# Kernel tuning notes

Hardware: AMD Instinct MI355X
Metric: run time of the kernel (lower is better)

## Reference

```python
import jax, jax.numpy as jnp
import numpy as np

NEG_BIG = -1e12
ALPHA = 0.2  # LeakyReLU negative slope

def setup_inputs() -> dict:
    key = jax.random.key(0)
    k1, k2, k3, k4, k5 = jax.random.split(key, 5)
    N, F_in, F_out = 8192, 256, 128
    inp = jax.random.normal(k1, (N, F_in), dtype=jnp.float32)
    adj = jax.random.randint(k2, (N, N), 0, 2, dtype=jnp.int32)
    W = jax.random.normal(k3, (F_in, F_out), dtype=jnp.float32) * 0.05
    W_2 = jax.random.normal(k4, (F_in, F_out), dtype=jnp.float32) * 0.05
    W_3 = jax.random.normal(k5, (F_in, F_out), dtype=jnp.float32) * 0.05
    return {"inp": inp, "adj": adj, "W": W, "W_2": W_2, "W_3": W_3}

def reference(inp, adj, W, W_2, W_3):
    # h = inp @ W, h_2 = inp @ W_2  -> scores e = LeakyReLU(h @ h_2^T)  [N, N]
    h = inp @ W
    h_2 = inp @ W_2
    e = jax.nn.leaky_relu(h @ h_2.T, negative_slope=ALPHA)
    # adjacency mask, row softmax (dropout disabled: eval mode)
    attention = jax.nn.softmax(jnp.where(adj > 0, e, NEG_BIG), axis=1)
    h_3 = inp @ W_3
    h_prime = attention @ h_3
    return jax.nn.elu(h_prime)  # concat=True path
```

## Files before the change

kernel.cpp:

```cpp
#include <hip/hip_runtime.h>
#include <hip/hip_fp16.h>

#define N    8192
#define FIN  256
#define FOUT 128
#define BN   64

typedef _Float16 half8 __attribute__((ext_vector_type(8)));
typedef _Float16 half4v __attribute__((ext_vector_type(4)));
typedef float floatx4 __attribute__((ext_vector_type(4)));

__global__ __launch_bounds__(256)
void wprep_kernel(const float* __restrict__ W0,
                  const float* __restrict__ W1,
                  const float* __restrict__ W2,
                  _Float16* __restrict__ Wf)
{
    int idx  = blockIdx.x * 256 + threadIdx.x;
    int lane = idx & 63;
    int frag = idx >> 6;
    int w    = frag >> 6;
    int f    = frag & 63;
    int nt   = f >> 3, kc = f & 7;
    int quad = lane >> 4, lo16 = lane & 15;
    const float* Wp = w == 0 ? W0 : (w == 1 ? W1 : W2);
    half8 v;
#pragma unroll
    for (int jj = 0; jj < 8; jj++)
        v[jj] = (_Float16)Wp[(size_t)(kc * 32 + quad * 8 + jj) * FOUT + nt * 16 + lo16];
    *(half8*)&Wf[(size_t)idx * 8] = v;
}

__global__ __launch_bounds__(256, 2)
void gemm3_kernel(const float* __restrict__ inp,
                  const _Float16* __restrict__ Wf,
                  _Float16* __restrict__ H,
                  _Float16* __restrict__ H2,
                  _Float16* __restrict__ H3T)
{
    const int which = blockIdx.z;
    const int c0    = blockIdx.y * 64;
    const _Float16* Wfw = Wf + (size_t)which * 64 * 64 * 8;
    const int r0 = blockIdx.x * 64;
    const int tid  = threadIdx.x;
    const int wave = tid >> 6;
    const int lane = tid & 63;
    const int lo16 = lane & 15;
    const int quad = lane >> 4;
    const int r = r0 + wave * 16 + lo16;

    half8 a[8];
#pragma unroll
    for (int kc = 0; kc < 8; kc++) {
        const float* p = &inp[(size_t)r * FIN + kc * 32 + quad * 8];
        float4 v0 = *(const float4*)p;
        float4 v1 = *(const float4*)(p + 4);
        a[kc][0] = (_Float16)v0.x; a[kc][1] = (_Float16)v0.y;
        a[kc][2] = (_Float16)v0.z; a[kc][3] = (_Float16)v0.w;
        a[kc][4] = (_Float16)v1.x; a[kc][5] = (_Float16)v1.y;
        a[kc][6] = (_Float16)v1.z; a[kc][7] = (_Float16)v1.w;
    }

    floatx4 acc[4];
#pragma unroll
    for (int i = 0; i < 4; i++) acc[i] = (floatx4){0.f, 0.f, 0.f, 0.f};

#pragma unroll
    for (int kc = 0; kc < 8; kc++)
#pragma unroll
        for (int nt = 0; nt < 4; nt++) {
            int ntg = (c0 >> 4) + nt;
            half8 b = *(const half8*)&Wfw[(((size_t)ntg * 8 + kc) * 64 + lane) * 8];
            acc[nt] = __builtin_amdgcn_mfma_f32_16x16x32_f16(a[kc], b, acc[nt], 0, 0, 0);
        }

    const int arow = wave * 16 + quad * 4;
    if (which < 2) {
        _Float16* outp = which == 0 ? H : H2;
#pragma unroll
        for (int nt = 0; nt < 4; nt++)
#pragma unroll
            for (int rr = 0; rr < 4; rr++)
                outp[(size_t)(r0 + arow + rr) * FOUT + c0 + nt * 16 + lo16] = (_Float16)acc[nt][rr];
    } else {
#pragma unroll
        for (int nt = 0; nt < 4; nt++) {
            half4v v;
#pragma unroll
            for (int rr = 0; rr < 4; rr++) v[rr] = (_Float16)acc[nt][rr];
            *(half4v*)&H3T[(size_t)(c0 + nt * 16 + lo16) * N + r0 + arow] = v;
        }
    }
}

__global__ __launch_bounds__(256)
void repackK_kernel(const _Float16* __restrict__ H2, _Float16* __restrict__ Kf)
{
    int idx  = blockIdx.x * 256 + threadIdx.x;
    int lane = idx & 63;
    int frag = idx >> 6;
    int jb = frag >> 4, f = frag & 15;
    int c = f >> 3, ntj = (f >> 2) & 1, kc = f & 3;
    int quad = lane >> 4, lo16 = lane & 15;
    int srcrow = jb * 64 + c * 32 + (lo16 >> 2) * 8 + ntj * 4 + (lo16 & 3);
    half8 v = *(const half8*)&H2[(size_t)srcrow * FOUT + kc * 32 + quad * 8];
    *(half8*)&Kf[(size_t)idx * 8] = v;
}

__global__ __launch_bounds__(256)
void repackV_kernel(const _Float16* __restrict__ H3T, _Float16* __restrict__ Vf)
{
    int idx  = blockIdx.x * 256 + threadIdx.x;
    int lane = idx & 63;
    int frag = idx >> 6;
    int jb = frag >> 4, f = frag & 15, nt = f >> 1, kc = f & 1;
    int quad = lane >> 4, lo16 = lane & 15;
    half8 v = *(const half8*)&H3T[(size_t)(nt * 16 + lo16) * N + jb * 64 + kc * 32 + quad * 8];
    *(half8*)&Vf[(size_t)idx * 8] = v;
}

template<int JS>
__global__ __launch_bounds__(256, 2)
void attn_kernel(const _Float16* __restrict__ Hq,
                 const _Float16* __restrict__ Kf,
                 const _Float16* __restrict__ Vf,
                 const int* __restrict__ adj,
                 float* __restrict__ OpartT,
                 float* __restrict__ mpart,
                 float* __restrict__ lpart)
{
    __shared__ _Float16 KV[2][16384];

    const int tid  = threadIdx.x;
    const int wave = tid >> 6;
    const int lane = tid & 63;
    const int lo16 = lane & 15;
    const int quad = lane >> 4;
    const int bid  = blockIdx.x;
    const int js   = bid & (JS - 1);
    const int ib   = bid / JS;
    const int i0   = ib * 128;
    const int iw   = i0 + wave * 32;
    const int jbeg = js * (N / JS);
    const int NIT  = (N / JS) / BN;

    half8 q[2][4];
#pragma unroll
    for (int isub = 0; isub < 2; isub++)
#pragma unroll
        for (int kc = 0; kc < 4; kc++)
            q[isub][kc] = *(const half8*)&Hq[(size_t)(iw + isub * 16 + lo16) * FOUT + kc * 32 + quad * 8];

    floatx4 O[8][2];
#pragma unroll
    for (int nt = 0; nt < 8; nt++)
#pragma unroll
        for (int s = 0; s < 2; s++) O[nt][s] = (floatx4){0.f, 0.f, 0.f, 0.f};
    float m_s[2] = {-1e12f, -1e12f}, l_s[2] = {0.f, 0.f};

    int av[32];
    {
        const int* ap = adj + (size_t)iw * N + jbeg + lane;
#pragma unroll
        for (int x = 0; x < 32; x++) av[x] = ap[(size_t)x * N];
    }

    {
        const int jb0 = jbeg >> 6;
        const _Float16* gk = Kf + (size_t)jb0 * 8192;
        const _Float16* gv = Vf + (size_t)jb0 * 8192;
#pragma unroll
        for (int r = 0; r < 4; r++) {
            int off = (r * 256 + tid) * 8;
            *(half8*)&KV[0][off]        = *(const half8*)&gk[off];
            *(half8*)&KV[0][8192 + off] = *(const half8*)&gv[off];
        }
        __syncthreads();
    }

    int cur = 0;
    for (int it = 0; it < NIT; it++) {
        const int j0 = jbeg + it * BN;

        unsigned long long mw0 = 0, mw1 = 0;
#pragma unroll
        for (int x = 0; x < 16; x++) {
            unsigned long long b0 = __ballot(av[x] != 0);
            unsigned long long b1 = __ballot(av[x + 16] != 0);
            bool sel = (lo16 == x);
            mw0 = sel ? b0 : mw0;
            mw1 = sel ? b1 : mw1;
        }
        unsigned long long mw[2] = {mw0, mw1};

        if (it + 1 < NIT) {
            const int* ap = adj + (size_t)iw * N + (j0 + BN) + lane;
#pragma unroll
            for (int x = 0; x < 32; x++) av[x] = ap[(size_t)x * N];
        }

        half8 st[8];
        if (it + 1 < NIT) {
            const int jbn = (j0 + BN) >> 6;
            const _Float16* gk = Kf + (size_t)jbn * 8192;
            const _Float16* gv = Vf + (size_t)jbn * 8192;
#pragma unroll
            for (int r = 0; r < 4; r++) {
                int off = (r * 256 + tid) * 8;
                st[r]     = *(const half8*)&gk[off];
                st[r + 4] = *(const half8*)&gv[off];
            }
        }

        const _Float16* kb = &KV[cur][0];
        const _Float16* vb = &KV[cur][8192];

        floatx4 S[2][2][2];
#pragma unroll
        for (int c = 0; c < 2; c++)
#pragma unroll
            for (int ntj = 0; ntj < 2; ntj++) {
                S[c][ntj][0] = (floatx4){0.f, 0.f, 0.f, 0.f};
                S[c][ntj][1] = (floatx4){0.f, 0.f, 0.f, 0.f};
#pragma unroll
                for (int kc = 0; kc < 4; kc++) {
                    half8 kf = *(const half8*)&kb[(((c * 2 + ntj) * 4 + kc) * 64 + lane) * 8];
                    S[c][ntj][0] = __builtin_amdgcn_mfma_f32_16x16x32_f16(kf, q[0][kc], S[c][ntj][0], 0, 0, 0);
                    S[c][ntj][1] = __builtin_amdgcn_mfma_f32_16x16x32_f16(kf, q[1][kc], S[c][ntj][1], 0, 0, 0);
                }
            }

        float alpha[2];
#pragma unroll
        for (int s = 0; s < 2; s++) {
            float mx = -1e12f;
#pragma unroll
            for (int c = 0; c < 2; c++)
#pragma unroll
                for (int ntj = 0; ntj < 2; ntj++)
#pragma unroll
                    for (int r = 0; r < 4; r++) {
                        float e = S[c][ntj][s][r];
                        e = e > 0.f ? e : 0.2f * e;
                        mx = fmaxf(mx, e);
                    }
            mx = fmaxf(mx, __shfl_xor(mx, 16));
            mx = fmaxf(mx, __shfl_xor(mx, 32));
            float mn = fmaxf(m_s[s], mx);
            alpha[s] = __expf(m_s[s] - mn);
            m_s[s] = mn;
        }

        half8 pb[2][2];
        float sum[2] = {0.f, 0.f};
#pragma unroll
        for (int s = 0; s < 2; s++) {
            unsigned long long mq = mw[s] >> (quad * 8);
#pragma unroll
            for (int c = 0; c < 2; c++)
#pragma unroll
                for (int ntj = 0; ntj < 2; ntj++)
#pragma unroll
                    for (int r = 0; r < 4; r++) {
                        float e = S[c][ntj][s][r];
                        e = e > 0.f ? e : 0.2f * e;
                        bool bit = (mq >> (c * 32 + ntj * 4 + r)) & 1ull;
                        float p = bit ? __expf(e - m_s[s]) : 0.f;
                        sum[s] += p;
                        pb[s][c][ntj * 4 + r] = (_Float16)p;
                    }
            sum[s] += __shfl_xor(sum[s], 16);
            sum[s] += __shfl_xor(sum[s], 32);
            l_s[s] = l_s[s] * alpha[s] + sum[s];
#pragma unroll
            for (int nt = 0; nt < 8; nt++)
#pragma unroll
                for (int r = 0; r < 4; r++)
                    O[nt][s][r] *= alpha[s];
        }

#pragma unroll
        for (int c = 0; c < 2; c++)
#pragma unroll
            for (int nt = 0; nt < 8; nt++) {
                half8 vf = *(const half8*)&vb[((nt * 2 + c) * 64 + lane) * 8];
                O[nt][0] = __builtin_amdgcn_mfma_f32_16x16x32_f16(vf, pb[0][c], O[nt][0], 0, 0, 0);
                O[nt][1] = __builtin_amdgcn_mfma_f32_16x16x32_f16(vf, pb[1][c], O[nt][1], 0, 0, 0);
            }

        if (it + 1 < NIT) {
            const int nxt = cur ^ 1;
#pragma unroll
            for (int r = 0; r < 4; r++) {
                int off = (r * 256 + tid) * 8;
                *(half8*)&KV[nxt][off]        = st[r];
                *(half8*)&KV[nxt][8192 + off] = st[r + 4];
            }
        }
        __syncthreads();
        cur ^= 1;
    }

#pragma unroll
    for (int nt = 0; nt < 8; nt++)
#pragma unroll
        for (int s = 0; s < 2; s++)
#pragma unroll
            for (int r = 0; r < 4; r++) {
                int f = nt * 16 + quad * 4 + r;
                int i = iw + s * 16 + lo16;
                OpartT[((size_t)js * FOUT + f) * N + i] = O[nt][s][r];
            }
    if (quad == 0) {
#pragma unroll
        for (int s = 0; s < 2; s++) {
            mpart[js * N + iw + s * 16 + lo16] = m_s[s];
            lpart[js * N + iw + s * 16 + lo16] = l_s[s];
        }
    }
}

template<int JS>
__global__ __launch_bounds__(256)
void combine_kernel(const float* __restrict__ OpartT,
                    const float* __restrict__ mpart,
                    const float* __restrict__ lpart,
                    float* __restrict__ out)
{
    int idx = blockIdx.x * 256 + threadIdx.x;
    int f  = idx >> 11;
    int i4 = (idx & 2047) << 2;

    float4 M = {-3e38f, -3e38f, -3e38f, -3e38f};
    float4 m[JS];
#pragma unroll
    for (int s = 0; s < JS; s++) {
        m[s] = *(const float4*)&mpart[s * N + i4];
        M.x = fmaxf(M.x, m[s].x); M.y = fmaxf(M.y, m[s].y);
        M.z = fmaxf(M.z, m[s].z); M.w = fmaxf(M.w, m[s].w);
    }
    float4 L = {0.f, 0.f, 0.f, 0.f};
    float4 w[JS];
#pragma unroll
    for (int s = 0; s < JS; s++) {
        float4 l = *(const float4*)&lpart[s * N + i4];
        w[s].x = __expf(m[s].x - M.x); w[s].y = __expf(m[s].y - M.y);
        w[s].z = __expf(m[s].z - M.z); w[s].w = __expf(m[s].w - M.w);
        L.x += l.x * w[s].x; L.y += l.y * w[s].y;
        L.z += l.z * w[s].z; L.w += l.w * w[s].w;
    }
    float4 o = {0.f, 0.f, 0.f, 0.f};
#pragma unroll
    for (int s = 0; s < JS; s++) {
        float4 v = *(const float4*)&OpartT[((size_t)s * FOUT + f) * N + i4];
        o.x += w[s].x * v.x; o.y += w[s].y * v.y;
        o.z += w[s].z * v.z; o.w += w[s].w * v.w;
    }
    float r0 = o.x / L.x, r1 = o.y / L.y, r2 = o.z / L.z, r3 = o.w / L.w;
    out[(size_t)(i4 + 0) * FOUT + f] = r0 > 0.f ? r0 : __expf(r0) - 1.f;
    out[(size_t)(i4 + 1) * FOUT + f] = r1 > 0.f ? r1 : __expf(r1) - 1.f;
    out[(size_t)(i4 + 2) * FOUT + f] = r2 > 0.f ? r2 : __expf(r2) - 1.f;
    out[(size_t)(i4 + 3) * FOUT + f] = r3 > 0.f ? r3 : __expf(r3) - 1.f;
}

extern "C" void kernel_launch(void* const* d_in, const int* in_sizes, int n_in,
                              void* d_out, int out_size, void* d_ws, size_t ws_size,
                              hipStream_t stream) {
    const float* inp = (const float*)d_in[0];
    const int*   adj = (const int*)d_in[1];
    const float* W0  = (const float*)d_in[2];
    const float* W1  = (const float*)d_in[3];
    const float* W2  = (const float*)d_in[4];
    float* out = (float*)d_out;

    constexpr int JS = 8;
    char* ws = (char*)d_ws;
    _Float16* H    = (_Float16*)(ws);
    _Float16* H2   = (_Float16*)(ws + (2u << 20));
    _Float16* H3T  = (_Float16*)(ws + (4u << 20));
    _Float16* Wf   = (_Float16*)(ws + (6u << 20));
    _Float16* Kf   = (_Float16*)(ws + (7u << 20));
    _Float16* Vf   = (_Float16*)(ws + (9u << 20));
    float* OpartT  = (float*)(ws + (11u << 20));
    float* mpart   = (float*)(ws + (43u << 20));
    float* lpart   = (float*)(ws + (43u << 20) + (size_t)JS * N * sizeof(float));

    wprep_kernel<<<48, 256, 0, stream>>>(W0, W1, W2, Wf);
    gemm3_kernel<<<dim3(N / 64, 2, 3), 256, 0, stream>>>(inp, Wf, H, H2, H3T);
    repackK_kernel<<<512, 256, 0, stream>>>(H2, Kf);
    repackV_kernel<<<512, 256, 0, stream>>>(H3T, Vf);
    attn_kernel<JS><<<(N / 128) * JS, 256, 0, stream>>>(H, Kf, Vf, adj, OpartT, mpart, lpart);
    combine_kernel<JS><<<(FOUT * (N / 4)) / 256, 256, 0, stream>>>(OpartT, mpart, lpart, out);
}
```

Baseline: 428.5 us.

## Split attention tile into two 32-column sub-steps and merge repack kernels

The attention inner loop now handles each 64-column key block as two 32-column halves. Each half runs its own online-softmax update and PV MFMA, so fewer score registers are live at once, which eases register pressure at two blocks per SM. The adjacency prefetch is moved after the K/V global loads, and the two repack kernels are merged into one launch. The cost is twice as many max/sum reductions and O rescales per block.

```diff
diff --git a/kernel.cpp b/kernel.cpp
--- a/kernel.cpp
+++ b/kernel.cpp
@@ -94,29 +94,30 @@
 }
 
 __global__ __launch_bounds__(256)
-void repackK_kernel(const _Float16* __restrict__ H2, _Float16* __restrict__ Kf)
-{
-    int idx  = blockIdx.x * 256 + threadIdx.x;
-    int lane = idx & 63;
-    int frag = idx >> 6;
-    int jb = frag >> 4, f = frag & 15;
-    int c = f >> 3, ntj = (f >> 2) & 1, kc = f & 3;
-    int quad = lane >> 4, lo16 = lane & 15;
-    int srcrow = jb * 64 + c * 32 + (lo16 >> 2) * 8 + ntj * 4 + (lo16 & 3);
-    half8 v = *(const half8*)&H2[(size_t)srcrow * FOUT + kc * 32 + quad * 8];
-    *(half8*)&Kf[(size_t)idx * 8] = v;
-}
-
-__global__ __launch_bounds__(256)
-void repackV_kernel(const _Float16* __restrict__ H3T, _Float16* __restrict__ Vf)
-{
-    int idx  = blockIdx.x * 256 + threadIdx.x;
-    int lane = idx & 63;
-    int frag = idx >> 6;
-    int jb = frag >> 4, f = frag & 15, nt = f >> 1, kc = f & 1;
-    int quad = lane >> 4, lo16 = lane & 15;
-    half8 v = *(const half8*)&H3T[(size_t)(nt * 16 + lo16) * N + jb * 64 + kc * 32 + quad * 8];
-    *(half8*)&Vf[(size_t)idx * 8] = v;
+void repackKV_kernel(const _Float16* __restrict__ H2,
+                     const _Float16* __restrict__ H3T,
+                     _Float16* __restrict__ Kf,
+                     _Float16* __restrict__ Vf)
+{
+    if (blockIdx.x < 512) {
+        int idx  = blockIdx.x * 256 + threadIdx.x;
+        int lane = idx & 63;
+        int frag = idx >> 6;
+        int jb = frag >> 4, f = frag & 15;
+        int c = f >> 3, ntj = (f >> 2) & 1, kc = f & 3;
+        int quad = lane >> 4, lo16 = lane & 15;
+        int srcrow = jb * 64 + c * 32 + (lo16 >> 2) * 8 + ntj * 4 + (lo16 & 3);
+        half8 v = *(const half8*)&H2[(size_t)srcrow * FOUT + kc * 32 + quad * 8];
+        *(half8*)&Kf[(size_t)idx * 8] = v;
+    } else {
+        int idx  = (blockIdx.x - 512) * 256 + threadIdx.x;
+        int lane = idx & 63;
+        int frag = idx >> 6;
+        int jb = frag >> 4, f = frag & 15, nt = f >> 1, kc = f & 1;
+        int quad = lane >> 4, lo16 = lane & 15;
+        half8 v = *(const half8*)&H3T[(size_t)(nt * 16 + lo16) * N + jb * 64 + kc * 32 + quad * 8];
+        *(half8*)&Vf[(size_t)idx * 8] = v;
+    }
 }
 
 template<int JS>
@@ -193,12 +194,6 @@
         }
         unsigned long long mw[2] = {mw0, mw1};
 
-        if (it + 1 < NIT) {
-            const int* ap = adj + (size_t)iw * N + (j0 + BN) + lane;
-#pragma unroll
-            for (int x = 0; x < 32; x++) av[x] = ap[(size_t)x * N];
-        }
-
         half8 st[8];
         if (it + 1 < NIT) {
             const int jbn = (j0 + BN) >> 6;
@@ -212,81 +207,82 @@
             }
         }
 
+        if (it + 1 < NIT) {
+            const int* ap = adj + (size_t)iw * N + (j0 + BN) + lane;
+#pragma unroll
+            for (int x = 0; x < 32; x++) av[x] = ap[(size_t)x * N];
+        }
+
         const _Float16* kb = &KV[cur][0];
         const _Float16* vb = &KV[cur][8192];
 
-        floatx4 S[2][2][2];
-#pragma unroll
-        for (int c = 0; c < 2; c++)
+#pragma unroll
+        for (int c = 0; c < 2; c++) {
+            floatx4 S[2][2];
 #pragma unroll
             for (int ntj = 0; ntj < 2; ntj++) {
-                S[c][ntj][0] = (floatx4){0.f, 0.f, 0.f, 0.f};
-                S[c][ntj][1] = (floatx4){0.f, 0.f, 0.f, 0.f};
+                S[ntj][0] = (floatx4){0.f, 0.f, 0.f, 0.f};
+                S[ntj][1] = (floatx4){0.f, 0.f, 0.f, 0.f};
 #pragma unroll
                 for (int kc = 0; kc < 4; kc++) {
                     half8 kf = *(const half8*)&kb[(((c * 2 + ntj) * 4 + kc) * 64 + lane) * 8];
-                    S[c][ntj][0] = __builtin_amdgcn_mfma_f32_16x16x32_f16(kf, q[0][kc], S[c][ntj][0], 0, 0, 0);
-                    S[c][ntj][1] = __builtin_amdgcn_mfma_f32_16x16x32_f16(kf, q[1][kc], S[c][ntj][1], 0, 0, 0);
+                    S[ntj][0] = __builtin_amdgcn_mfma_f32_16x16x32_f16(kf, q[0][kc], S[ntj][0], 0, 0, 0);
+                    S[ntj][1] = __builtin_amdgcn_mfma_f32_16x16x32_f16(kf, q[1][kc], S[ntj][1], 0, 0, 0);
                 }
             }
 
-        float alpha[2];
-#pragma unroll
-        for (int s = 0; s < 2; s++) {
-            float mx = -1e12f;
-#pragma unroll
-            for (int c = 0; c < 2; c++)
+            float alpha[2];
+#pragma unroll
+            for (int s = 0; s < 2; s++) {
+                float mx = -1e12f;
 #pragma unroll
                 for (int ntj = 0; ntj < 2; ntj++)
 #pragma unroll
                     for (int r = 0; r < 4; r++) {
-                        float e = S[c][ntj][s][r];
+                        float e = S[ntj][s][r];
                         e = e > 0.f ? e : 0.2f * e;
                         mx = fmaxf(mx, e);
                     }
-            mx = fmaxf(mx, __shfl_xor(mx, 16));
-            mx = fmaxf(mx, __shfl_xor(mx, 32));
-            float mn = fmaxf(m_s[s], mx);
-            alpha[s] = __expf(m_s[s] - mn);
-            m_s[s] = mn;
-        }
-
-        half8 pb[2][2];
-        float sum[2] = {0.f, 0.f};
-#pragma unroll
-        for (int s = 0; s < 2; s++) {
-            unsigned long long mq = mw[s] >> (quad * 8);
-#pragma unroll
-            for (int c = 0; c < 2; c++)
+                mx = fmaxf(mx, __shfl_xor(mx, 16));
+                mx = fmaxf(mx, __shfl_xor(mx, 32));
+                float mn = fmaxf(m_s[s], mx);
+                alpha[s] = __expf(m_s[s] - mn);
+                m_s[s] = mn;
+            }
+
+            half8 pb[2];
+            float sum[2] = {0.f, 0.f};
+#pragma unroll
+            for (int s = 0; s < 2; s++) {
+                unsigned long long mq = mw[s] >> (quad * 8 + c * 32);
 #pragma unroll
                 for (int ntj = 0; ntj < 2; ntj++)
 #pragma unroll
                     for (int r = 0; r < 4; r++) {
-                        float e = S[c][ntj][s][r];
+                        float e = S[ntj][s][r];
                         e = e > 0.f ? e : 0.2f * e;
-                        bool bit = (mq >> (c * 32 + ntj * 4 + r)) & 1ull;
+                        bool bit = (mq >> (ntj * 4 + r)) & 1ull;
                         float p = bit ? __expf(e - m_s[s]) : 0.f;
                         sum[s] += p;
-                        pb[s][c][ntj * 4 + r] = (_Float16)p;
+                        pb[s][ntj * 4 + r] = (_Float16)p;
                     }
-            sum[s] += __shfl_xor(sum[s], 16);
-            sum[s] += __shfl_xor(sum[s], 32);
-            l_s[s] = l_s[s] * alpha[s] + sum[s];
-#pragma unroll
-            for (int nt = 0; nt < 8; nt++)
-#pragma unroll
-                for (int r = 0; r < 4; r++)
-                    O[nt][s][r] *= alpha[s];
-        }
-
-#pragma unroll
-        for (int c = 0; c < 2; c++)
+                sum[s] += __shfl_xor(sum[s], 16);
+                sum[s] += __shfl_xor(sum[s], 32);
+                l_s[s] = l_s[s] * alpha[s] + sum[s];
+#pragma unroll
+                for (int nt = 0; nt < 8; nt++)
+#pragma unroll
+                    for (int r = 0; r < 4; r++)
+                        O[nt][s][r] *= alpha[s];
+            }
+
 #pragma unroll
             for (int nt = 0; nt < 8; nt++) {
                 half8 vf = *(const half8*)&vb[((nt * 2 + c) * 64 + lane) * 8];
-                O[nt][0] = __builtin_amdgcn_mfma_f32_16x16x32_f16(vf, pb[0][c], O[nt][0], 0, 0, 0);
-                O[nt][1] = __builtin_amdgcn_mfma_f32_16x16x32_f16(vf, pb[1][c], O[nt][1], 0, 0, 0);
-            }
+                O[nt][0] = __builtin_amdgcn_mfma_f32_16x16x32_f16(vf, pb[0], O[nt][0], 0, 0, 0);
+                O[nt][1] = __builtin_amdgcn_mfma_f32_16x16x32_f16(vf, pb[1], O[nt][1], 0, 0, 0);
+            }
+        }
 
         if (it + 1 < NIT) {
             const int nxt = cur ^ 1;
@@ -387,8 +383,7 @@
 
     wprep_kernel<<<48, 256, 0, stream>>>(W0, W1, W2, Wf);
     gemm3_kernel<<<dim3(N / 64, 2, 3), 256, 0, stream>>>(inp, Wf, H, H2, H3T);
-    repackK_kernel<<<512, 256, 0, stream>>>(H2, Kf);
-    repackV_kernel<<<512, 256, 0, stream>>>(H3T, Vf);
+    repackKV_kernel<<<1024, 256, 0, stream>>>(H2, H3T, Kf, Vf);
     attn_kernel<JS><<<(N / 128) * JS, 256, 0, stream>>>(H, Kf, Vf, adj, OpartT, mpart, lpart);
     combine_kernel<JS><<<(FOUT * (N / 4)) / 256, 256, 0, stream>>>(OpartT, mpart, lpart, out);
 }
```

Measured after the change: 448.9 us. 1.05x slower.

## Drop LDS staging of K/V tiles, load fragments directly from global; merge repack kernels

Applied to the files above, without the earlier changes.

The attention kernel no longer double-buffers K/V tiles through shared memory with a per-iteration barrier. Each wave now reads its pre-packed K and V MFMA fragments straight from global memory, relying on L2/cache hits because all four waves read the same tile. The two repack kernels are also merged into one launch. This removes LDS traffic and block-wide syncs and may raise occupancy, but it adds redundant global/L2 loads per wave and more register pressure from holding 16 K fragments.

```diff
diff --git a/kernel.cpp b/kernel.cpp
--- a/kernel.cpp
+++ b/kernel.cpp
@@ -94,29 +94,30 @@
 }
 
 __global__ __launch_bounds__(256)
-void repackK_kernel(const _Float16* __restrict__ H2, _Float16* __restrict__ Kf)
-{
-    int idx  = blockIdx.x * 256 + threadIdx.x;
-    int lane = idx & 63;
-    int frag = idx >> 6;
-    int jb = frag >> 4, f = frag & 15;
-    int c = f >> 3, ntj = (f >> 2) & 1, kc = f & 3;
-    int quad = lane >> 4, lo16 = lane & 15;
-    int srcrow = jb * 64 + c * 32 + (lo16 >> 2) * 8 + ntj * 4 + (lo16 & 3);
-    half8 v = *(const half8*)&H2[(size_t)srcrow * FOUT + kc * 32 + quad * 8];
-    *(half8*)&Kf[(size_t)idx * 8] = v;
-}
-
-__global__ __launch_bounds__(256)
-void repackV_kernel(const _Float16* __restrict__ H3T, _Float16* __restrict__ Vf)
-{
-    int idx  = blockIdx.x * 256 + threadIdx.x;
-    int lane = idx & 63;
-    int frag = idx >> 6;
-    int jb = frag >> 4, f = frag & 15, nt = f >> 1, kc = f & 1;
-    int quad = lane >> 4, lo16 = lane & 15;
-    half8 v = *(const half8*)&H3T[(size_t)(nt * 16 + lo16) * N + jb * 64 + kc * 32 + quad * 8];
-    *(half8*)&Vf[(size_t)idx * 8] = v;
+void repackKV_kernel(const _Float16* __restrict__ H2,
+                     const _Float16* __restrict__ H3T,
+                     _Float16* __restrict__ Kf,
+                     _Float16* __restrict__ Vf)
+{
+    if (blockIdx.x < 512) {
+        int idx  = blockIdx.x * 256 + threadIdx.x;
+        int lane = idx & 63;
+        int frag = idx >> 6;
+        int jb = frag >> 4, f = frag & 15;
+        int c = f >> 3, ntj = (f >> 2) & 1, kc = f & 3;
+        int quad = lane >> 4, lo16 = lane & 15;
+        int srcrow = jb * 64 + c * 32 + (lo16 >> 2) * 8 + ntj * 4 + (lo16 & 3);
+        half8 v = *(const half8*)&H2[(size_t)srcrow * FOUT + kc * 32 + quad * 8];
+        *(half8*)&Kf[(size_t)idx * 8] = v;
+    } else {
+        int idx  = (blockIdx.x - 512) * 256 + threadIdx.x;
+        int lane = idx & 63;
+        int frag = idx >> 6;
+        int jb = frag >> 4, f = frag & 15, nt = f >> 1, kc = f & 1;
+        int quad = lane >> 4, lo16 = lane & 15;
+        half8 v = *(const half8*)&H3T[(size_t)(nt * 16 + lo16) * N + jb * 64 + kc * 32 + quad * 8];
+        *(half8*)&Vf[(size_t)idx * 8] = v;
+    }
 }
 
 template<int JS>
@@ -129,8 +130,6 @@
                  float* __restrict__ mpart,
                  float* __restrict__ lpart)
 {
-    __shared__ _Float16 KV[2][16384];
-
     const int tid  = threadIdx.x;
     const int wave = tid >> 6;
     const int lane = tid & 63;
@@ -139,8 +138,7 @@
     const int bid  = blockIdx.x;
     const int js   = bid & (JS - 1);
     const int ib   = bid / JS;
-    const int i0   = ib * 128;
-    const int iw   = i0 + wave * 32;
+    const int iw   = ib * 128 + wave * 32;
     const int jbeg = js * (N / JS);
     const int NIT  = (N / JS) / BN;
 
@@ -165,22 +163,11 @@
         for (int x = 0; x < 32; x++) av[x] = ap[(size_t)x * N];
     }
 
-    {
-        const int jb0 = jbeg >> 6;
-        const _Float16* gk = Kf + (size_t)jb0 * 8192;
-        const _Float16* gv = Vf + (size_t)jb0 * 8192;
-#pragma unroll
-        for (int r = 0; r < 4; r++) {
-            int off = (r * 256 + tid) * 8;
-            *(half8*)&KV[0][off]        = *(const half8*)&gk[off];
-            *(half8*)&KV[0][8192 + off] = *(const half8*)&gv[off];
-        }
-        __syncthreads();
-    }
-
-    int cur = 0;
     for (int it = 0; it < NIT; it++) {
         const int j0 = jbeg + it * BN;
+        const int jb = j0 >> 6;
+        const _Float16* gk = Kf + (size_t)jb * 8192;
+        const _Float16* gv = Vf + (size_t)jb * 8192;
 
         unsigned long long mw0 = 0, mw1 = 0;
 #pragma unroll
@@ -193,27 +180,16 @@
         }
         unsigned long long mw[2] = {mw0, mw1};
 
+        half8 kf[16];
+#pragma unroll
+        for (int f = 0; f < 16; f++)
+            kf[f] = *(const half8*)&gk[((size_t)f * 64 + lane) * 8];
+
         if (it + 1 < NIT) {
             const int* ap = adj + (size_t)iw * N + (j0 + BN) + lane;
 #pragma unroll
             for (int x = 0; x < 32; x++) av[x] = ap[(size_t)x * N];
         }
-
-        half8 st[8];
-        if (it + 1 < NIT) {
-            const int jbn = (j0 + BN) >> 6;
-            const _Float16* gk = Kf + (size_t)jbn * 8192;
-            const _Float16* gv = Vf + (size_t)jbn * 8192;
-#pragma unroll
-            for (int r = 0; r < 4; r++) {
-                int off = (r * 256 + tid) * 8;
-                st[r]     = *(const half8*)&gk[off];
-                st[r + 4] = *(const half8*)&gv[off];
-            }
-        }
-
-        const _Float16* kb = &KV[cur][0];
-        const _Float16* vb = &KV[cur][8192];
 
         floatx4 S[2][2][2];
 #pragma unroll
@@ -224,9 +200,9 @@
                 S[c][ntj][1] = (floatx4){0.f, 0.f, 0.f, 0.f};
 #pragma unroll
                 for (int kc = 0; kc < 4; kc++) {
-                    half8 kf = *(const half8*)&kb[(((c * 2 + ntj) * 4 + kc) * 64 + lane) * 8];
-                    S[c][ntj][0] = __builtin_amdgcn_mfma_f32_16x16x32_f16(kf, q[0][kc], S[c][ntj][0], 0, 0, 0);
-                    S[c][ntj][1] = __builtin_amdgcn_mfma_f32_16x16x32_f16(kf, q[1][kc], S[c][ntj][1], 0, 0, 0);
+                    half8 k8 = kf[(c * 2 + ntj) * 4 + kc];
+                    S[c][ntj][0] = __builtin_amdgcn_mfma_f32_16x16x32_f16(k8, q[0][kc], S[c][ntj][0], 0, 0, 0);
+                    S[c][ntj][1] = __builtin_amdgcn_mfma_f32_16x16x32_f16(k8, q[1][kc], S[c][ntj][1], 0, 0, 0);
                 }
             }
 
@@ -283,22 +259,10 @@
         for (int c = 0; c < 2; c++)
 #pragma unroll
             for (int nt = 0; nt < 8; nt++) {
-                half8 vf = *(const half8*)&vb[((nt * 2 + c) * 64 + lane) * 8];
+                half8 vf = *(const half8*)&gv[(((size_t)nt * 2 + c) * 64 + lane) * 8];
                 O[nt][0] = __builtin_amdgcn_mfma_f32_16x16x32_f16(vf, pb[0][c], O[nt][0], 0, 0, 0);
                 O[nt][1] = __builtin_amdgcn_mfma_f32_16x16x32_f16(vf, pb[1][c], O[nt][1], 0, 0, 0);
             }
-
-        if (it + 1 < NIT) {
-            const int nxt = cur ^ 1;
-#pragma unroll
-            for (int r = 0; r < 4; r++) {
-                int off = (r * 256 + tid) * 8;
-                *(half8*)&KV[nxt][off]        = st[r];
-                *(half8*)&KV[nxt][8192 + off] = st[r + 4];
-            }
-        }
-        __syncthreads();
-        cur ^= 1;
     }
 
 #pragma unroll
@@ -387,8 +351,7 @@
 
     wprep_kernel<<<48, 256, 0, stream>>>(W0, W1, W2, Wf);
     gemm3_kernel<<<dim3(N / 64, 2, 3), 256, 0, stream>>>(inp, Wf, H, H2, H3T);
-    repackK_kernel<<<512, 256, 0, stream>>>(H2, Kf);
-    repackV_kernel<<<512, 256, 0, stream>>>(H3T, Vf);
+    repackKV_kernel<<<1024, 256, 0, stream>>>(H2, H3T, Kf, Vf);
     attn_kernel<JS><<<(N / 128) * JS, 256, 0, stream>>>(H, Kf, Vf, adj, OpartT, mpart, lpart);
     combine_kernel<JS><<<(FOUT * (N / 4)) / 256, 256, 0, stream>>>(OpartT, mpart, lpart, out);
 }
```

New measurement: 448.3 us. +4.6%, slower.
